# Optimization experiments

Measured on AMD Instinct MI355X. Metric: run time of the kernel, lower is better.

Reference implementation:

```python
import jax, jax.numpy as jnp
import numpy as np

N_NODES = 50000
N_EDGES = 1_600_000
D = 64        # node/edge feature dim
RBF = 9       # radial basis degree
DIN = 3 * D   # concat(vi, vj, e)


def _gated_mlp(x, l1w, l1b, l2w, l2b, g1w, g1b, g2w, g2b):
    # layers branch: SiLU on every layer (activate_last=True)
    h = jax.nn.silu(x @ l1w.T + l1b)
    h = jax.nn.silu(h @ l2w.T + l2b)
    # gates branch: SiLU on hidden, sigmoid on last
    g = jax.nn.silu(x @ g1w.T + g1b)
    g = jax.nn.sigmoid(g @ g2w.T + g2b)
    return h * g


def setup_inputs() -> dict:
    key = jax.random.key(0)
    ks = jax.random.split(key, 24)
    s = 0.05
    inp = {
        "node_feat": jax.random.normal(ks[0], (N_NODES, D), jnp.float32),
        "edge_feat": jax.random.normal(ks[1], (N_EDGES, D), jnp.float32),
        "rbf": jax.random.normal(ks[2], (N_EDGES, RBF), jnp.float32),
        "src": jax.random.randint(ks[3], (N_EDGES,), 0, N_NODES, jnp.int32),
        "dst": jax.random.randint(ks[4], (N_EDGES,), 0, N_NODES, jnp.int32),
        # edge GatedMLP params
        "e_l1_w": jax.random.normal(ks[5], (D, DIN)) * s,  "e_l1_b": jnp.zeros((D,)),
        "e_l2_w": jax.random.normal(ks[6], (D, D)) * s,    "e_l2_b": jnp.zeros((D,)),
        "e_g1_w": jax.random.normal(ks[7], (D, DIN)) * s,  "e_g1_b": jnp.zeros((D,)),
        "e_g2_w": jax.random.normal(ks[8], (D, D)) * s,    "e_g2_b": jnp.zeros((D,)),
        # node GatedMLP params
        "n_l1_w": jax.random.normal(ks[9], (D, DIN)) * s,  "n_l1_b": jnp.zeros((D,)),
        "n_l2_w": jax.random.normal(ks[10], (D, D)) * s,   "n_l2_b": jnp.zeros((D,)),
        "n_g1_w": jax.random.normal(ks[11], (D, DIN)) * s, "n_g1_b": jnp.zeros((D,)),
        "n_g2_w": jax.random.normal(ks[12], (D, D)) * s,   "n_g2_b": jnp.zeros((D,)),
        # rbf -> weight linear projections (bias=False)
        "edge_w_w": jax.random.normal(ks[13], (D, RBF)) * s,
        "node_w_w": jax.random.normal(ks[14], (D, RBF)) * s,
    }
    return inp


def reference(node_feat, edge_feat, rbf, src, dst,
              e_l1_w, e_l1_b, e_l2_w, e_l2_b, e_g1_w, e_g1_b, e_g2_w, e_g2_b,
              n_l1_w, n_l1_b, n_l2_w, n_l2_b, n_g1_w, n_g1_b, n_g2_w, n_g2_b,
              edge_w_w, node_w_w):
    vi = node_feat[src]   # [E, D] gather src node features
    vj = node_feat[dst]   # [E, D] gather dst node features

    # ---- edge update: GatedMLP(concat) * Linear(rbf) ----
    x_e = jnp.concatenate([vi, vj, edge_feat], axis=1)  # [E, 3D]
    edge_update = _gated_mlp(x_e, e_l1_w, e_l1_b, e_l2_w, e_l2_b,
                             e_g1_w, e_g1_b, e_g2_w, e_g2_b) * (rbf @ edge_w_w.T)
    e_new = edge_feat + edge_update

    # ---- node update: per-edge message then scatter-sum to dst ----
    x_n = jnp.concatenate([vi, vj, e_new], axis=1)  # uses updated edge features
    mess = _gated_mlp(x_n, n_l1_w, n_l1_b, n_l2_w, n_l2_b,
                      n_g1_w, n_g1_b, n_g2_w, n_g2_b) * (rbf @ node_w_w.T)
    ve = jax.ops.segment_sum(mess, dst, num_segments=N_NODES)  # [N, D]
    v_new = node_feat + ve

    return e_new, v_new
```

## Files before the change

### kernel.cpp

```cpp
#include <hip/hip_runtime.h>

#define TILE_E 128

typedef __attribute__((ext_vector_type(8))) short bf16x8;
typedef __attribute__((ext_vector_type(4))) float f32x4;

__device__ __forceinline__ unsigned int f2bf(float f) {
    union { float f; unsigned int u; } v; v.f = f;
    return (v.u + 0x7FFFu + ((v.u >> 16) & 1u)) >> 16;
}
__device__ __forceinline__ float fsigmoid(float x) { return 1.0f / (1.0f + __expf(-x)); }
__device__ __forceinline__ float fsilu(float x) { return x * fsigmoid(x); }

#define O_EL1 0
#define O_EG1 12288
#define O_EL2 24576
#define O_EG2 28672
#define O_NL1 32768
#define O_NG1 45056
#define O_NL2 57344
#define O_NG2 61440

__global__ void prep_weights(const float* el1, const float* eg1, const float* el2, const float* eg2,
                             const float* nl1, const float* ng1, const float* nl2, const float* ng2,
                             unsigned short* wout) {
    int tid = blockIdx.x * 256 + threadIdx.x;
    if (tid >= 65536) return;
    int idx = tid; const float* s; int base, K;
    if (idx < 12288)      { s = el1; base = O_EL1; K = 192; }
    else if (idx < 24576) { idx -= 12288; s = eg1; base = O_EG1; K = 192; }
    else if (idx < 28672) { idx -= 24576; s = el2; base = O_EL2; K = 64; }
    else if (idx < 32768) { idx -= 28672; s = eg2; base = O_EG2; K = 64; }
    else if (idx < 45056) { idx -= 32768; s = nl1; base = O_NL1; K = 192; }
    else if (idx < 57344) { idx -= 45056; s = ng1; base = O_NG1; K = 192; }
    else if (idx < 61440) { idx -= 57344; s = nl2; base = O_NL2; K = 64; }
    else                  { idx -= 61440; s = ng2; base = O_NG2; K = 64; }
    int n = (K == 192) ? (idx / 192) : (idx >> 6);
    int k = idx - n * K;
    int off = (((n >> 4) * (K >> 5) + (k >> 5)) * 4 + ((k >> 3) & 3)) * 128 + ((n & 15) << 3) + (k & 7);
    wout[base + off] = (unsigned short)f2bf(s[idx]);
}

__global__ void vinit(const float* __restrict__ node_feat, float* __restrict__ out_v, int n) {
    int i = blockIdx.x * 256 + threadIdx.x;
    if (i < n) out_v[i] = node_feat[i];
}

__device__ __forceinline__ void gated_mlp(
    const unsigned short* __restrict__ Xw, unsigned short* __restrict__ HGw,
    const unsigned short* __restrict__ wb,
    int oL1, int oL2, int oG1, int oG2,
    const float* __restrict__ bL1, const float* __restrict__ bL2,
    const float* __restrict__ bG1, const float* __restrict__ bG2,
    int lane, f32x4 prod[2][4])
{
    const int qp = lane >> 4, ln = lane & 15;

    bf16x8 a1[2][6];
    #pragma unroll
    for (int rt = 0; rt < 2; ++rt)
        #pragma unroll
        for (int t = 0; t < 6; ++t)
            a1[rt][t] = *(const bf16x8*)(Xw + rt * 3072 + t * 512 + lane * 8);

    f32x4 acc2h[2][4], acc2g[2][4];

    #pragma unroll
    for (int br = 0; br < 2; ++br) {
        const int o1 = br ? oG1 : oL1;
        const int o2 = br ? oG2 : oL2;
        const float* b1 = br ? bG1 : bL1;

        f32x4 acc[2][4];
        #pragma unroll
        for (int rt = 0; rt < 2; ++rt)
            #pragma unroll
            for (int nt = 0; nt < 4; ++nt)
                acc[rt][nt] = (f32x4){0.f, 0.f, 0.f, 0.f};
        #pragma unroll
        for (int nt = 0; nt < 4; ++nt)
            #pragma unroll
            for (int t = 0; t < 6; ++t) {
                bf16x8 bfr = *(const bf16x8*)(wb + o1 + (nt * 6 + t) * 512 + lane * 8);
                acc[0][nt] = __builtin_amdgcn_mfma_f32_16x16x32_bf16(a1[0][t], bfr, acc[0][nt], 0, 0, 0);
                acc[1][nt] = __builtin_amdgcn_mfma_f32_16x16x32_bf16(a1[1][t], bfr, acc[1][nt], 0, 0, 0);
            }
        #pragma unroll
        for (int nt = 0; nt < 4; ++nt) {
            const float bias = b1[nt * 16 + ln];
            const int f = nt * 16 + ln, t2 = f >> 5, q2 = (f >> 3) & 3, j2 = f & 7;
            #pragma unroll
            for (int rt = 0; rt < 2; ++rt)
                #pragma unroll
                for (int r = 0; r < 4; ++r) {
                    float v = fsilu(acc[rt][nt][r] + bias);
                    HGw[rt * 1024 + t2 * 512 + q2 * 128 + (qp * 4 + r) * 8 + j2] = (unsigned short)f2bf(v);
                }
        }
        asm volatile("s_waitcnt lgkmcnt(0)" ::: "memory");

        bf16x8 a2[2][2];
        #pragma unroll
        for (int rt = 0; rt < 2; ++rt)
            #pragma unroll
            for (int t2 = 0; t2 < 2; ++t2)
                a2[rt][t2] = *(const bf16x8*)(HGw + rt * 1024 + t2 * 512 + lane * 8);

        f32x4 (*acc2)[4] = br ? acc2g : acc2h;
        #pragma unroll
        for (int rt = 0; rt < 2; ++rt)
            #pragma unroll
            for (int nt = 0; nt < 4; ++nt)
                acc2[rt][nt] = (f32x4){0.f, 0.f, 0.f, 0.f};
        #pragma unroll
        for (int nt = 0; nt < 4; ++nt)
            #pragma unroll
            for (int t2 = 0; t2 < 2; ++t2) {
                bf16x8 bfr = *(const bf16x8*)(wb + o2 + (nt * 2 + t2) * 512 + lane * 8);
                acc2[0][nt] = __builtin_amdgcn_mfma_f32_16x16x32_bf16(a2[0][t2], bfr, acc2[0][nt], 0, 0, 0);
                acc2[1][nt] = __builtin_amdgcn_mfma_f32_16x16x32_bf16(a2[1][t2], bfr, acc2[1][nt], 0, 0, 0);
            }
    }

    #pragma unroll
    for (int nt = 0; nt < 4; ++nt) {
        const float b2v = bL2[nt * 16 + ln], bg2v = bG2[nt * 16 + ln];
        #pragma unroll
        for (int rt = 0; rt < 2; ++rt)
            #pragma unroll
            for (int r = 0; r < 4; ++r)
                prod[rt][nt][r] = fsilu(acc2h[rt][nt][r] + b2v) * fsigmoid(acc2g[rt][nt][r] + bg2v);
    }
}

__global__ __launch_bounds__(256, 2) void m3g_main(
    const float* __restrict__ node_feat, const float* __restrict__ edge_feat,
    const float* __restrict__ rbf, const int* __restrict__ src, const int* __restrict__ dst,
    const unsigned short* __restrict__ wb,
    const float* __restrict__ el1b, const float* __restrict__ el2b,
    const float* __restrict__ eg1b, const float* __restrict__ eg2b,
    const float* __restrict__ nl1b, const float* __restrict__ nl2b,
    const float* __restrict__ ng1b, const float* __restrict__ ng2b,
    const float* __restrict__ eww, const float* __restrict__ nww,
    float* __restrict__ out_e, float* __restrict__ out_v, int E)
{
    __shared__ unsigned short Xs[128 * 192];
    __shared__ unsigned short HGs[4 * 2048];
    __shared__ float rbfs[128 * 9];
    __shared__ float ews[576];
    __shared__ float nws[576];
    __shared__ int dsts[128];

    const int tid = threadIdx.x;
    const int e0 = blockIdx.x * TILE_E;

    if (tid < 128) { int eg = e0 + tid; dsts[tid] = (eg < E) ? dst[eg] : 0; }
    for (int i = tid; i < 1152; i += 256) { int gi = e0 * 9 + i; rbfs[i] = (gi < E * 9) ? rbf[gi] : 0.0f; }
    for (int i = tid; i < 576; i += 256) { ews[i] = eww[i]; nws[i] = nww[i]; }

    {
        const int el = tid >> 1, cb = (tid & 1) * 32;
        const int eg = min(e0 + el, E - 1);
        const int reg = el >> 4;
        const int m = el & 15;
        const float* r0 = node_feat + (size_t)src[eg] * 64;
        const float* r1 = node_feat + (size_t)dst[eg] * 64;
        const float* r2 = edge_feat + (size_t)eg * 64;
        const float* rows[3] = { r0, r1, r2 };
        #pragma unroll
        for (int s = 0; s < 3; ++s) {
            const float4* rp = (const float4*)(rows[s] + cb);
            #pragma unroll
            for (int o = 0; o < 4; ++o) {
                float4 f0 = rp[o * 2], f1 = rp[o * 2 + 1];
                uint4 u;
                u.x = f2bf(f0.x) | (f2bf(f0.y) << 16);
                u.y = f2bf(f0.z) | (f2bf(f0.w) << 16);
                u.z = f2bf(f1.x) | (f2bf(f1.y) << 16);
                u.w = f2bf(f1.z) | (f2bf(f1.w) << 16);
                int kk = s * 64 + cb + o * 8;
                int t = kk >> 5, q = (kk >> 3) & 3;
                *(uint4*)&Xs[reg * 3072 + (t * 4 + q) * 128 + m * 8] = u;
            }
        }
    }
    __syncthreads();

    const int w = tid >> 6, lane = tid & 63;
    const int qp = lane >> 4, ln = lane & 15;
    const unsigned short* Xw = Xs + w * 2 * 3072;
    unsigned short* HGw = HGs + w * 2048;

    f32x4 prodE[2][4];
    gated_mlp(Xw, HGw, wb, O_EL1, O_EL2, O_EG1, O_EG2, el1b, el2b, eg1b, eg2b, lane, prodE);

    float ewv[4][9];
    #pragma unroll
    for (int nt = 0; nt < 4; ++nt)
        #pragma unroll
        for (int ri = 0; ri < 9; ++ri)
            ewv[nt][ri] = ews[(nt * 16 + ln) * 9 + ri];

    #pragma unroll
    for (int rt = 0; rt < 2; ++rt)
        #pragma unroll
        for (int r = 0; r < 4; ++r) {
            const int m = qp * 4 + r, el = w * 32 + rt * 16 + m, eg = e0 + el;
            float rb[9];
            #pragma unroll
            for (int ri = 0; ri < 9; ++ri) rb[ri] = rbfs[el * 9 + ri];
            if (eg < E) {
                #pragma unroll
                for (int nt = 0; nt < 4; ++nt) {
                    float rw = 0.0f;
                    #pragma unroll
                    for (int ri = 0; ri < 9; ++ri) rw += rb[ri] * ewv[nt][ri];
                    const int f = nt * 16 + ln;
                    float en = edge_feat[(size_t)eg * 64 + f] + prodE[rt][nt][r] * rw;
                    out_e[(size_t)eg * 64 + f] = en;
                    const int kk = 128 + f, t = kk >> 5, q = (kk >> 3) & 3;
                    Xs[(w * 2 + rt) * 3072 + (t * 4 + q) * 128 + m * 8 + (f & 7)] = (unsigned short)f2bf(en);
                }
            }
        }
    asm volatile("s_waitcnt lgkmcnt(0)" ::: "memory");

    f32x4 prodN[2][4];
    gated_mlp(Xw, HGw, wb, O_NL1, O_NL2, O_NG1, O_NG2, nl1b, nl2b, ng1b, ng2b, lane, prodN);

    float nwv[4][9];
    #pragma unroll
    for (int nt = 0; nt < 4; ++nt)
        #pragma unroll
        for (int ri = 0; ri < 9; ++ri)
            nwv[nt][ri] = nws[(nt * 16 + ln) * 9 + ri];

    #pragma unroll
    for (int rt = 0; rt < 2; ++rt)
        #pragma unroll
        for (int r = 0; r < 4; ++r) {
            const int m = qp * 4 + r, el = w * 32 + rt * 16 + m, eg = e0 + el;
            float rb[9];
            #pragma unroll
            for (int ri = 0; ri < 9; ++ri) rb[ri] = rbfs[el * 9 + ri];
            if (eg < E) {
                const int dn = dsts[el];
                #pragma unroll
                for (int nt = 0; nt < 4; ++nt) {
                    float rw = 0.0f;
                    #pragma unroll
                    for (int ri = 0; ri < 9; ++ri) rw += rb[ri] * nwv[nt][ri];
                    float mess = prodN[rt][nt][r] * rw;
                    unsafeAtomicAdd(&out_v[(size_t)dn * 64 + nt * 16 + ln], mess);
                }
            }
        }
}

extern "C" void kernel_launch(void* const* d_in, const int* in_sizes, int n_in,
                              void* d_out, int out_size, void* d_ws, size_t ws_size,
                              hipStream_t stream) {
    const float* node_feat = (const float*)d_in[0];
    const float* edge_feat = (const float*)d_in[1];
    const float* rbf  = (const float*)d_in[2];
    const int*   src  = (const int*)d_in[3];
    const int*   dst  = (const int*)d_in[4];
    const float* el1w = (const float*)d_in[5];
    const float* el1b = (const float*)d_in[6];
    const float* el2w = (const float*)d_in[7];
    const float* el2b = (const float*)d_in[8];
    const float* eg1w = (const float*)d_in[9];
    const float* eg1b = (const float*)d_in[10];
    const float* eg2w = (const float*)d_in[11];
    const float* eg2b = (const float*)d_in[12];
    const float* nl1w = (const float*)d_in[13];
    const float* nl1b = (const float*)d_in[14];
    const float* nl2w = (const float*)d_in[15];
    const float* nl2b = (const float*)d_in[16];
    const float* ng1w = (const float*)d_in[17];
    const float* ng1b = (const float*)d_in[18];
    const float* ng2w = (const float*)d_in[19];
    const float* ng2b = (const float*)d_in[20];
    const float* eww  = (const float*)d_in[21];
    const float* nww  = (const float*)d_in[22];

    const int E = in_sizes[1] / 64;
    const int N = in_sizes[0] / 64;
    float* out_e = (float*)d_out;
    float* out_v = out_e + (size_t)E * 64;
    unsigned short* wbf = (unsigned short*)d_ws;

    prep_weights<<<256, 256, 0, stream>>>(el1w, eg1w, el2w, eg2w, nl1w, ng1w, nl2w, ng2w, wbf);
    vinit<<<(N * 64 + 255) / 256, 256, 0, stream>>>(node_feat, out_v, N * 64);
    m3g_main<<<(E + TILE_E - 1) / TILE_E, 256, 0, stream>>>(
        node_feat, edge_feat, rbf, src, dst, wbf,
        el1b, el2b, eg1b, eg2b, nl1b, nl2b, ng1b, ng2b,
        eww, nww, out_e, out_v, E);
}
```

Before: 1.583 ms.

## Use 512-thread blocks with one 16-edge tile per wave and packed bf16 conversion

Each wave now handles 16 edges instead of 32, so blocks grow to 512 threads (8 waves) and per-wave registers roughly halve, with launch bounds asking for 4 blocks per CU. The rbf and projection-weight tables are no longer staged in LDS and are read directly from global memory, which cuts LDS use and the staging work. Float-to-bf16 conversion switches to the hardware v_cvt_pk_bf16_f32 instruction. The aim is more latency hiding through higher occupancy. The cost is less reuse of each weight fragment per MFMA and extra uncached-style global loads for rbf.

```diff
diff --git a/kernel.cpp b/kernel.cpp
--- a/kernel.cpp
+++ b/kernel.cpp
@@ -8,6 +8,11 @@
 __device__ __forceinline__ unsigned int f2bf(float f) {
     union { float f; unsigned int u; } v; v.f = f;
     return (v.u + 0x7FFFu + ((v.u >> 16) & 1u)) >> 16;
+}
+__device__ __forceinline__ unsigned int cvt_pk_bf16(float lo, float hi) {
+    unsigned int r;
+    asm("v_cvt_pk_bf16_f32 %0, %1, %2" : "=v"(r) : "v"(lo), "v"(hi));
+    return r;
 }
 __device__ __forceinline__ float fsigmoid(float x) { return 1.0f / (1.0f + __expf(-x)); }
 __device__ __forceinline__ float fsilu(float x) { return x * fsigmoid(x); }
@@ -52,18 +57,16 @@
     int oL1, int oL2, int oG1, int oG2,
     const float* __restrict__ bL1, const float* __restrict__ bL2,
     const float* __restrict__ bG1, const float* __restrict__ bG2,
-    int lane, f32x4 prod[2][4])
+    int lane, f32x4 prod[4])
 {
     const int qp = lane >> 4, ln = lane & 15;
 
-    bf16x8 a1[2][6];
-    #pragma unroll
-    for (int rt = 0; rt < 2; ++rt)
-        #pragma unroll
-        for (int t = 0; t < 6; ++t)
-            a1[rt][t] = *(const bf16x8*)(Xw + rt * 3072 + t * 512 + lane * 8);
-
-    f32x4 acc2h[2][4], acc2g[2][4];
+    bf16x8 a1[6];
+    #pragma unroll
+    for (int t = 0; t < 6; ++t)
+        a1[t] = *(const bf16x8*)(Xw + t * 512 + lane * 8);
+
+    f32x4 acc2h[4], acc2g[4];
 
     #pragma unroll
     for (int br = 0; br < 2; ++br) {
@@ -71,54 +74,47 @@
         const int o2 = br ? oG2 : oL2;
         const float* b1 = br ? bG1 : bL1;
 
-        f32x4 acc[2][4];
-        #pragma unroll
-        for (int rt = 0; rt < 2; ++rt)
-            #pragma unroll
-            for (int nt = 0; nt < 4; ++nt)
-                acc[rt][nt] = (f32x4){0.f, 0.f, 0.f, 0.f};
+        f32x4 acc[4];
+        #pragma unroll
+        for (int nt = 0; nt < 4; ++nt)
+            acc[nt] = (f32x4){0.f, 0.f, 0.f, 0.f};
         #pragma unroll
         for (int nt = 0; nt < 4; ++nt)
             #pragma unroll
             for (int t = 0; t < 6; ++t) {
                 bf16x8 bfr = *(const bf16x8*)(wb + o1 + (nt * 6 + t) * 512 + lane * 8);
-                acc[0][nt] = __builtin_amdgcn_mfma_f32_16x16x32_bf16(a1[0][t], bfr, acc[0][nt], 0, 0, 0);
-                acc[1][nt] = __builtin_amdgcn_mfma_f32_16x16x32_bf16(a1[1][t], bfr, acc[1][nt], 0, 0, 0);
+                acc[nt] = __builtin_amdgcn_mfma_f32_16x16x32_bf16(a1[t], bfr, acc[nt], 0, 0, 0);
             }
         #pragma unroll
         for (int nt = 0; nt < 4; ++nt) {
             const float bias = b1[nt * 16 + ln];
             const int f = nt * 16 + ln, t2 = f >> 5, q2 = (f >> 3) & 3, j2 = f & 7;
-            #pragma unroll
-            for (int rt = 0; rt < 2; ++rt)
-                #pragma unroll
-                for (int r = 0; r < 4; ++r) {
-                    float v = fsilu(acc[rt][nt][r] + bias);
-                    HGw[rt * 1024 + t2 * 512 + q2 * 128 + (qp * 4 + r) * 8 + j2] = (unsigned short)f2bf(v);
-                }
+            unsigned short* hp = HGw + t2 * 512 + q2 * 128 + j2;
+            #pragma unroll
+            for (int r2 = 0; r2 < 4; r2 += 2) {
+                unsigned int p = cvt_pk_bf16(fsilu(acc[nt][r2] + bias),
+                                             fsilu(acc[nt][r2 + 1] + bias));
+                hp[(qp * 4 + r2) * 8]     = (unsigned short)p;
+                hp[(qp * 4 + r2 + 1) * 8] = (unsigned short)(p >> 16);
+            }
         }
         asm volatile("s_waitcnt lgkmcnt(0)" ::: "memory");
 
-        bf16x8 a2[2][2];
-        #pragma unroll
-        for (int rt = 0; rt < 2; ++rt)
-            #pragma unroll
-            for (int t2 = 0; t2 < 2; ++t2)
-                a2[rt][t2] = *(const bf16x8*)(HGw + rt * 1024 + t2 * 512 + lane * 8);
-
-        f32x4 (*acc2)[4] = br ? acc2g : acc2h;
-        #pragma unroll
-        for (int rt = 0; rt < 2; ++rt)
-            #pragma unroll
-            for (int nt = 0; nt < 4; ++nt)
-                acc2[rt][nt] = (f32x4){0.f, 0.f, 0.f, 0.f};
+        bf16x8 a2[2];
+        #pragma unroll
+        for (int t2 = 0; t2 < 2; ++t2)
+            a2[t2] = *(const bf16x8*)(HGw + t2 * 512 + lane * 8);
+
+        f32x4* acc2 = br ? acc2g : acc2h;
+        #pragma unroll
+        for (int nt = 0; nt < 4; ++nt)
+            acc2[nt] = (f32x4){0.f, 0.f, 0.f, 0.f};
         #pragma unroll
         for (int nt = 0; nt < 4; ++nt)
             #pragma unroll
             for (int t2 = 0; t2 < 2; ++t2) {
                 bf16x8 bfr = *(const bf16x8*)(wb + o2 + (nt * 2 + t2) * 512 + lane * 8);
-                acc2[0][nt] = __builtin_amdgcn_mfma_f32_16x16x32_bf16(a2[0][t2], bfr, acc2[0][nt], 0, 0, 0);
-                acc2[1][nt] = __builtin_amdgcn_mfma_f32_16x16x32_bf16(a2[1][t2], bfr, acc2[1][nt], 0, 0, 0);
+                acc2[nt] = __builtin_amdgcn_mfma_f32_16x16x32_bf16(a2[t2], bfr, acc2[nt], 0, 0, 0);
             }
     }
 
@@ -126,14 +122,12 @@
     for (int nt = 0; nt < 4; ++nt) {
         const float b2v = bL2[nt * 16 + ln], bg2v = bG2[nt * 16 + ln];
         #pragma unroll
-        for (int rt = 0; rt < 2; ++rt)
-            #pragma unroll
-            for (int r = 0; r < 4; ++r)
-                prod[rt][nt][r] = fsilu(acc2h[rt][nt][r] + b2v) * fsigmoid(acc2g[rt][nt][r] + bg2v);
-    }
-}
-
-__global__ __launch_bounds__(256, 2) void m3g_main(
+        for (int r = 0; r < 4; ++r)
+            prod[nt][r] = fsilu(acc2h[nt][r] + b2v) * fsigmoid(acc2g[nt][r] + bg2v);
+    }
+}
+
+__global__ __launch_bounds__(512, 4) void m3g_main(
     const float* __restrict__ node_feat, const float* __restrict__ edge_feat,
     const float* __restrict__ rbf, const int* __restrict__ src, const int* __restrict__ dst,
     const unsigned short* __restrict__ wb,
@@ -145,21 +139,16 @@
     float* __restrict__ out_e, float* __restrict__ out_v, int E)
 {
     __shared__ unsigned short Xs[128 * 192];
-    __shared__ unsigned short HGs[4 * 2048];
-    __shared__ float rbfs[128 * 9];
-    __shared__ float ews[576];
-    __shared__ float nws[576];
+    __shared__ unsigned short HGs[8 * 1024];
     __shared__ int dsts[128];
 
     const int tid = threadIdx.x;
     const int e0 = blockIdx.x * TILE_E;
 
     if (tid < 128) { int eg = e0 + tid; dsts[tid] = (eg < E) ? dst[eg] : 0; }
-    for (int i = tid; i < 1152; i += 256) { int gi = e0 * 9 + i; rbfs[i] = (gi < E * 9) ? rbf[gi] : 0.0f; }
-    for (int i = tid; i < 576; i += 256) { ews[i] = eww[i]; nws[i] = nww[i]; }
 
     {
-        const int el = tid >> 1, cb = (tid & 1) * 32;
+        const int el = tid >> 2, cb = (tid & 3) * 16;
         const int eg = min(e0 + el, E - 1);
         const int reg = el >> 4;
         const int m = el & 15;
@@ -171,13 +160,13 @@
         for (int s = 0; s < 3; ++s) {
             const float4* rp = (const float4*)(rows[s] + cb);
             #pragma unroll
-            for (int o = 0; o < 4; ++o) {
+            for (int o = 0; o < 2; ++o) {
                 float4 f0 = rp[o * 2], f1 = rp[o * 2 + 1];
                 uint4 u;
-                u.x = f2bf(f0.x) | (f2bf(f0.y) << 16);
-                u.y = f2bf(f0.z) | (f2bf(f0.w) << 16);
-                u.z = f2bf(f1.x) | (f2bf(f1.y) << 16);
-                u.w = f2bf(f1.z) | (f2bf(f1.w) << 16);
+                u.x = cvt_pk_bf16(f0.x, f0.y);
+                u.y = cvt_pk_bf16(f0.z, f0.w);
+                u.z = cvt_pk_bf16(f1.x, f1.y);
+                u.w = cvt_pk_bf16(f1.z, f1.w);
                 int kk = s * 64 + cb + o * 8;
                 int t = kk >> 5, q = (kk >> 3) & 3;
                 *(uint4*)&Xs[reg * 3072 + (t * 4 + q) * 128 + m * 8] = u;
@@ -188,10 +177,10 @@
 
     const int w = tid >> 6, lane = tid & 63;
     const int qp = lane >> 4, ln = lane & 15;
-    const unsigned short* Xw = Xs + w * 2 * 3072;
-    unsigned short* HGw = HGs + w * 2048;
-
-    f32x4 prodE[2][4];
+    const unsigned short* Xw = Xs + w * 3072;
+    unsigned short* HGw = HGs + w * 1024;
+
+    f32x4 prodE[4];
     gated_mlp(Xw, HGw, wb, O_EL1, O_EL2, O_EG1, O_EG2, el1b, el2b, eg1b, eg2b, lane, prodE);
 
     float ewv[4][9];
@@ -199,33 +188,31 @@
     for (int nt = 0; nt < 4; ++nt)
         #pragma unroll
         for (int ri = 0; ri < 9; ++ri)
-            ewv[nt][ri] = ews[(nt * 16 + ln) * 9 + ri];
-
-    #pragma unroll
-    for (int rt = 0; rt < 2; ++rt)
-        #pragma unroll
-        for (int r = 0; r < 4; ++r) {
-            const int m = qp * 4 + r, el = w * 32 + rt * 16 + m, eg = e0 + el;
+            ewv[nt][ri] = eww[(nt * 16 + ln) * 9 + ri];
+
+    #pragma unroll
+    for (int r = 0; r < 4; ++r) {
+        const int m = qp * 4 + r, el = w * 16 + m, eg = e0 + el;
+        if (eg < E) {
             float rb[9];
             #pragma unroll
-            for (int ri = 0; ri < 9; ++ri) rb[ri] = rbfs[el * 9 + ri];
-            if (eg < E) {
+            for (int ri = 0; ri < 9; ++ri) rb[ri] = rbf[(size_t)eg * 9 + ri];
+            #pragma unroll
+            for (int nt = 0; nt < 4; ++nt) {
+                float rw = 0.0f;
                 #pragma unroll
-                for (int nt = 0; nt < 4; ++nt) {
-                    float rw = 0.0f;
-                    #pragma unroll
-                    for (int ri = 0; ri < 9; ++ri) rw += rb[ri] * ewv[nt][ri];
-                    const int f = nt * 16 + ln;
-                    float en = edge_feat[(size_t)eg * 64 + f] + prodE[rt][nt][r] * rw;
-                    out_e[(size_t)eg * 64 + f] = en;
-                    const int kk = 128 + f, t = kk >> 5, q = (kk >> 3) & 3;
-                    Xs[(w * 2 + rt) * 3072 + (t * 4 + q) * 128 + m * 8 + (f & 7)] = (unsigned short)f2bf(en);
-                }
-            }
-        }
+                for (int ri = 0; ri < 9; ++ri) rw += rb[ri] * ewv[nt][ri];
+                const int f = nt * 16 + ln;
+                float en = edge_feat[(size_t)eg * 64 + f] + prodE[nt][r] * rw;
+                out_e[(size_t)eg * 64 + f] = en;
+                const int kk = 128 + f, t = kk >> 5, q = (kk >> 3) & 3;
+                Xs[w * 3072 + (t * 4 + q) * 128 + m * 8 + (f & 7)] = (unsigned short)f2bf(en);
+            }
+        }
+    }
     asm volatile("s_waitcnt lgkmcnt(0)" ::: "memory");
 
-    f32x4 prodN[2][4];
+    f32x4 prodN[4];
     gated_mlp(Xw, HGw, wb, O_NL1, O_NL2, O_NG1, O_NG2, nl1b, nl2b, ng1b, ng2b, lane, prodN);
 
     float nwv[4][9];
@@ -233,28 +220,26 @@
     for (int nt = 0; nt < 4; ++nt)
         #pragma unroll
         for (int ri = 0; ri < 9; ++ri)
-            nwv[nt][ri] = nws[(nt * 16 + ln) * 9 + ri];
-
-    #pragma unroll
-    for (int rt = 0; rt < 2; ++rt)
-        #pragma unroll
-        for (int r = 0; r < 4; ++r) {
-            const int m = qp * 4 + r, el = w * 32 + rt * 16 + m, eg = e0 + el;
+            nwv[nt][ri] = nww[(nt * 16 + ln) * 9 + ri];
+
+    #pragma unroll
+    for (int r = 0; r < 4; ++r) {
+        const int m = qp * 4 + r, el = w * 16 + m, eg = e0 + el;
+        if (eg < E) {
             float rb[9];
             #pragma unroll
-            for (int ri = 0; ri < 9; ++ri) rb[ri] = rbfs[el * 9 + ri];
-            if (eg < E) {
-                const int dn = dsts[el];
+            for (int ri = 0; ri < 9; ++ri) rb[ri] = rbf[(size_t)eg * 9 + ri];
+            const int dn = dsts[el];
+            #pragma unroll
+            for (int nt = 0; nt < 4; ++nt) {
+                float rw = 0.0f;
                 #pragma unroll
-                for (int nt = 0; nt < 4; ++nt) {
-                    float rw = 0.0f;
-                    #pragma unroll
-                    for (int ri = 0; ri < 9; ++ri) rw += rb[ri] * nwv[nt][ri];
-                    float mess = prodN[rt][nt][r] * rw;
-                    unsafeAtomicAdd(&out_v[(size_t)dn * 64 + nt * 16 + ln], mess);
-                }
-            }
-        }
+                for (int ri = 0; ri < 9; ++ri) rw += rb[ri] * nwv[nt][ri];
+                float mess = prodN[nt][r] * rw;
+                unsafeAtomicAdd(&out_v[(size_t)dn * 64 + nt * 16 + ln], mess);
+            }
+        }
+    }
 }
 
 extern "C" void kernel_launch(void* const* d_in, const int* in_sizes, int n_in,
@@ -292,7 +277,7 @@
 
     prep_weights<<<256, 256, 0, stream>>>(el1w, eg1w, el2w, eg2w, nl1w, ng1w, nl2w, ng2w, wbf);
     vinit<<<(N * 64 + 255) / 256, 256, 0, stream>>>(node_feat, out_v, N * 64);
-    m3g_main<<<(E + TILE_E - 1) / TILE_E, 256, 0, stream>>>(
+    m3g_main<<<(E + TILE_E - 1) / TILE_E, 512, 0, stream>>>(
         node_feat, edge_feat, rbf, src, dst, wbf,
         el1b, el2b, eg1b, eg2b, nl1b, nl2b, ng1b, ng2b,
         eww, nww, out_e, out_v, E);
```

Measured after the change: 1.456 ms. 1.09x faster.
